# Kernel tuning notes

Measured on AMD Instinct MI355X. Metric: run time of the kernel, lower is better.

## Reference

```python
import jax, jax.numpy as jnp
import numpy as np
import math

C_S, C_Z, H, D, P_QK, P_V = 384, 128, 12, 16, 4, 8
B, L = 1, 512

def setup_inputs() -> dict:
    ks = jax.random.split(jax.random.key(0), 16)
    sc = lambda fan_in: 1.0 / math.sqrt(fan_in)
    return {
        's': jax.random.normal(ks[0], (B, L, C_S), jnp.float32),
        'z': jax.random.normal(ks[1], (B, L, L, C_Z), jnp.float32),
        'R': jax.random.normal(ks[2], (B, L, 3, 3), jnp.float32),
        't': jax.random.normal(ks[3], (B, L, 3), jnp.float32),
        'g_s': jnp.ones((C_S,), jnp.float32),
        'b_s': jnp.zeros((C_S,), jnp.float32),
        'g_z': jnp.ones((C_Z,), jnp.float32),
        'b_z': jnp.zeros((C_Z,), jnp.float32),
        'Wq': jax.random.normal(ks[4], (C_S, H * D), jnp.float32) * sc(C_S),
        'Wk': jax.random.normal(ks[5], (C_S, H * D), jnp.float32) * sc(C_S),
        'Wv': jax.random.normal(ks[6], (C_S, H * D), jnp.float32) * sc(C_S),
        'Wqp': jax.random.normal(ks[7], (C_S, H * P_QK * 3), jnp.float32) * sc(C_S),
        'Wkp': jax.random.normal(ks[8], (C_S, H * P_QK * 3), jnp.float32) * sc(C_S),
        'Wvp': jax.random.normal(ks[9], (C_S, H * P_V * 3), jnp.float32) * sc(C_S),
        'Wpb': jax.random.normal(ks[10], (C_Z, H), jnp.float32) * sc(C_Z),
        'pw': jax.random.normal(ks[11], (H,), jnp.float32) * 0.1,
        'Wo': jax.random.normal(ks[12], (H * D + H * P_V * 3 + H * P_V, C_S), jnp.float32) * sc(H * D + H * P_V * 3 + H * P_V),
        'bo': jnp.zeros((C_S,), jnp.float32),
    }

def _ln(x, g, b, eps=1e-5):
    mu = jnp.mean(x, axis=-1, keepdims=True)
    var = jnp.mean(jnp.square(x - mu), axis=-1, keepdims=True)
    return (x - mu) * jax.lax.rsqrt(var + eps) * g + b

def reference(s, z, R, t, g_s, b_s, g_z, b_z, Wq, Wk, Wv, Wqp, Wkp, Wvp, Wpb, pw, Wo, bo):
    Bn, Ln, _ = s.shape
    sn = _ln(s, g_s, b_s)
    zn = _ln(z, g_z, b_z)
    q_s = (sn @ Wq).reshape(Bn, Ln, H, D)
    k_s = (sn @ Wk).reshape(Bn, Ln, H, D)
    v_s = (sn @ Wv).reshape(Bn, Ln, H, D)
    q_pl = (sn @ Wqp).reshape(Bn, Ln, H, P_QK, 3)
    k_pl = (sn @ Wkp).reshape(Bn, Ln, H, P_QK, 3)
    v_pl = (sn @ Wvp).reshape(Bn, Ln, H, P_V, 3)
    # local->global frame transform: x_global = R x_local + t
    tb = t[:, :, None, None, :]
    q_p = jnp.einsum('blij,blhpj->blhpi', R, q_pl) + tb
    k_p = jnp.einsum('blij,blhpj->blhpi', R, k_pl) + tb
    v_p = jnp.einsum('blij,blhpj->blhpi', R, v_pl) + tb
    scalar_logits = jnp.einsum('bihd,bjhd->bijh', q_s, k_s) / math.sqrt(D)
    pair_logits = zn @ Wpb  # (B,L,L,H)
    # sum_p |q_ip - k_jp|^2 without materializing the (B,L,L,H,P,3) diff tensor
    qn2 = jnp.sum(jnp.square(q_p), axis=(-1, -2))  # (B,L,H)
    kn2 = jnp.sum(jnp.square(k_p), axis=(-1, -2))
    qk = jnp.einsum('bihpc,bjhpc->bijh', q_p, k_p)
    dist2 = qn2[:, :, None, :] + kn2[:, None, :, :] - 2.0 * qk
    w = jax.nn.softplus(pw)[None, None, None, :]
    logits = scalar_logits + pair_logits - 0.5 * w * dist2
    attn = jax.nn.softmax(logits, axis=2)  # over keys j
    out_s = jnp.einsum('bijh,bjhd->bihd', attn, v_s)
    out_pg = jnp.einsum('bijh,bjhpc->bihpc', attn, v_p)
    # global->local: R^T (x - t); (R^T)_{xy} = R_{yx}
    out_pl = jnp.einsum('blyx,blhpy->blhpx', R, out_pg - tb)
    out_pn = jnp.sqrt(jnp.sum(jnp.square(out_pl), axis=-1) + 1e-8)
    out_cat = jnp.concatenate([out_s.reshape(Bn, Ln, -1), out_pl.reshape(Bn, Ln, -1), out_pn.reshape(Bn, Ln, -1)], axis=-1)
    return s + out_cat @ Wo + bo
```

## Files before the change

kernel.cpp:

```cpp
#include <hip/hip_runtime.h>

typedef float f32x4 __attribute__((ext_vector_type(4)));
typedef short bf16x8 __attribute__((ext_vector_type(8)));
typedef unsigned short u16x4 __attribute__((ext_vector_type(4)));

#define MFMA16(a,b,c) __builtin_amdgcn_mfma_f32_16x16x32_bf16((a),(b),(c),0,0,0)

__device__ __forceinline__ unsigned short f2bf(float f){
  unsigned int u = __builtin_bit_cast(unsigned int, f);
  u += 0x7FFFu + ((u>>16)&1u);
  return (unsigned short)(u>>16);
}
__device__ __forceinline__ float bf2f(unsigned short u){
  return __builtin_bit_cast(float, ((unsigned int)u)<<16);
}

#define OFF_SNBF  0u
#define OFF_PROJ  393216u
#define OFF_QP    2752512u
#define OFF_KFRAG 3047424u
#define OFF_VFRAG 3440640u
#define OFF_KN2   4030464u
#define OFF_PLT   4055040u
#define OFF_OBUF  10346496u
#define OFF_CATBF 11329536u
#define OFF_WPBF  11919360u
#define OFF_GZF   11923456u
#define OFF_BZF   11931648u
#define OFF_WCF   11939840u
#define OFF_WOF   12824576u
#define OFF_WBUF  13266944u

__global__ __launch_bounds__(256) void k_prep(
    const float* __restrict__ s, const float* __restrict__ g_s, const float* __restrict__ b_s,
    unsigned short* __restrict__ snbf,
    const float* __restrict__ Wq, const float* __restrict__ Wk, const float* __restrict__ Wv,
    const float* __restrict__ Wqp, const float* __restrict__ Wkp, const float* __restrict__ Wvp,
    const float* __restrict__ Wpb, const float* __restrict__ pw, const float* __restrict__ Wo,
    const float* __restrict__ g_z, const float* __restrict__ b_z,
    unsigned short* __restrict__ wpbfrag, float* __restrict__ gzfrag, float* __restrict__ bzfrag,
    unsigned short* __restrict__ wcfrag, unsigned short* __restrict__ wofrag,
    float* __restrict__ wbuf){
  if (blockIdx.x < 128){
    int l = blockIdx.x*4 + (threadIdx.x>>6);
    int lane = threadIdx.x & 63;
    float v[6]; float sum=0.f, ss=0.f;
    #pragma unroll
    for (int k=0;k<6;k++){
      float x = s[l*384 + lane + 64*k];
      v[k]=x; sum += x; ss = fmaf(x,x,ss);
    }
    #pragma unroll
    for (int m=1;m<64;m<<=1){ sum += __shfl_xor(sum,m); ss += __shfl_xor(ss,m); }
    float mu = sum*(1.f/384.f);
    float var = ss*(1.f/384.f) - mu*mu;
    float rs = rsqrtf(var + 1e-5f);
    #pragma unroll
    for (int k=0;k<6;k++){
      int c = lane + 64*k;
      snbf[l*384 + c] = f2bf((v[k]-mu)*rs*g_s[c] + b_s[c]);
    }
    return;
  }
  int idx = (blockIdx.x-128)*256 + threadIdx.x;
  const int N_wpb = 2048, N_gz = 2048, N_wc = 72*12*64*8, N_wo = 24*18*64*8;
  if (idx < N_wpb){
    int r = idx&7, lane=(idx>>3)&63, chunk=idx>>9;
    int c = chunk*32 + ((lane>>4)<<3) + r; int h = lane&15;
    wpbfrag[idx] = (h<12) ? f2bf(Wpb[c*12+h]) : (unsigned short)0;
    return;
  }
  idx -= N_wpb;
  if (idx < N_gz){
    int r = idx&7, lane=(idx>>3)&63, chunk=idx>>9;
    int c = chunk*32 + ((lane>>4)<<3) + r;
    gzfrag[idx] = g_z[c]; bzfrag[idx] = b_z[c];
    return;
  }
  idx -= N_gz;
  if (idx < N_wc){
    int r = idx&7, lane=(idx>>3)&63, kt=(idx>>9)%12, nt=idx/(12*512);
    int k = kt*32 + ((lane>>4)<<3) + r; int n = nt*16 + (lane&15);
    float v;
    if      (n < 192) v = Wq [k*192 + n];
    else if (n < 384) v = Wk [k*192 + (n-192)];
    else if (n < 576) v = Wv [k*192 + (n-384)];
    else if (n < 720) v = Wqp[k*144 + (n-576)];
    else if (n < 864) v = Wkp[k*144 + (n-720)];
    else              v = Wvp[k*288 + (n-864)];
    wcfrag[idx] = f2bf(v);
    return;
  }
  idx -= N_wc;
  if (idx < N_wo){
    int r = idx&7, lane=(idx>>3)&63, kt=(idx>>9)%18, nt=idx/(18*512);
    int k = kt*32 + ((lane>>4)<<3) + r; int n = nt*16 + (lane&15);
    wofrag[idx] = f2bf(Wo[k*384 + n]);
    return;
  }
  idx -= N_wo;
  if (idx < 12){
    float x = pw[idx];
    wbuf[idx] = log1pf(expf(x));
  }
}

__global__ __launch_bounds__(256) void k_proj(const unsigned short* __restrict__ snbf,
    const unsigned short* __restrict__ wcfrag, float* __restrict__ proj){
  int wid = blockIdx.x*4 + (threadIdx.x>>6);
  int lane = threadIdx.x & 63;
  int il = lane&15, ig = lane>>4;
  int nt = wid % 72, ib = wid / 72;
  int i0 = ib*16;
  f32x4 acc = {0.f,0.f,0.f,0.f};
  #pragma unroll
  for (int kt=0; kt<12; kt++){
    bf16x8 a = *(const bf16x8*)(snbf + (i0+il)*384 + kt*32 + ig*8);
    bf16x8 b = *(const bf16x8*)(wcfrag + (size_t)((nt*12+kt)*64 + lane)*8);
    acc = MFMA16(a, b, acc);
  }
  #pragma unroll
  for (int r=0;r<4;r++)
    proj[(i0 + ig*4 + r)*1152 + nt*16 + il] = acc[r];
}

__global__ __launch_bounds__(192) void k_points(const float* __restrict__ proj,
    const float* __restrict__ Rm, const float* __restrict__ tv,
    float* __restrict__ qpb, unsigned short* __restrict__ kfrag,
    unsigned short* __restrict__ vfrag, float* __restrict__ kn2T){
  int l = blockIdx.x; int t = threadIdx.x;
  __shared__ float Rl[9], tl[3];
  __shared__ float kp_lds[12][12];
  __shared__ float vp_lds[12][24];
  __shared__ float kn2acc[12][4];
  if (t < 9) Rl[t] = Rm[l*9 + t];
  if (t < 3) tl[t] = tv[l*3 + t];
  __syncthreads();
  int h = t >> 4, pt = t & 15;
  {
    int ptype = (pt<4)? 0 : ((pt<8)? 1 : 2);
    int p = pt - ((ptype==0)?0:((ptype==1)?4:8));
    int col0 = (ptype==0)?576:((ptype==1)?720:864);
    int stride = (ptype==2)?24:12;
    const float* src = proj + l*1152 + col0 + h*stride + p*3;
    float lx=src[0], ly=src[1], lz=src[2];
    float cx = Rl[0]*lx + Rl[1]*ly + Rl[2]*lz + tl[0];
    float cy = Rl[3]*lx + Rl[4]*ly + Rl[5]*lz + tl[1];
    float cz = Rl[6]*lx + Rl[7]*ly + Rl[8]*lz + tl[2];
    if (ptype==0){
      float* d = qpb + (l*12 + h)*12 + p*3;
      d[0]=cx; d[1]=cy; d[2]=cz;
    } else if (ptype==1){
      kp_lds[h][p*3+0]=cx; kp_lds[h][p*3+1]=cy; kp_lds[h][p*3+2]=cz;
      kn2acc[h][p] = cx*cx + cy*cy + cz*cz;
    } else {
      vp_lds[h][p*3+0]=cx; vp_lds[h][p*3+1]=cy; vp_lds[h][p*3+2]=cz;
    }
  }
  __syncthreads();
  if (t < 12)
    kn2T[t*512 + l] = kn2acc[t][0]+kn2acc[t][1]+kn2acc[t][2]+kn2acc[t][3];
  {
    int jt = l >> 4, jl = l & 15;
    int q = pt >> 2, rr = (pt & 3)*2;
    unsigned short* dst = kfrag + (size_t)((h*32 + jt)*64 + 16*q + jl)*8 + rr;
    #pragma unroll
    for (int e=0;e<2;e++){
      int k = pt*2 + e; float f;
      if (k < 16)      f = proj[l*1152 + 192 + h*16 + k];
      else if (k < 28) f = kp_lds[h][k-16];
      else             f = 0.f;
      dst[e] = f2bf(f);
    }
  }
  {
    int d = pt; int jc = l >> 5; int jin = l & 31;
    int qq = (jin & 15) >> 2;
    int rr = (jin & 3) + ((jin >> 4) << 2);
    #pragma unroll
    for (int dt=0; dt<3; dt++){
      int dd = dt*16 + d; float f;
      if (dd < 16)      f = proj[l*1152 + 384 + h*16 + dd];
      else if (dd < 40) f = vp_lds[h][dd-16];
      else              f = 0.f;
      vfrag[(size_t)(((h*16 + jc)*3 + dt)*64 + 16*qq + d)*8 + rr] = f2bf(f);
    }
  }
}

__global__ __launch_bounds__(256) void k_pairbias(const float* __restrict__ z,
    const unsigned short* __restrict__ wpbfrag, const float* __restrict__ gzfrag,
    const float* __restrict__ bzfrag, unsigned short* __restrict__ plTbf){
  int w = blockIdx.x*4 + (threadIdx.x>>6);
  int lane = threadIdx.x & 63;
  int il = lane & 15, ig = lane >> 4;
  int nw = gridDim.x*4;
  f32x4 gzv[8], bzv[8];
  bf16x8 wf[4];
  #pragma unroll
  for (int c=0;c<4;c++){
    gzv[2*c]   = *(const f32x4*)(gzfrag + (c*64+lane)*8);
    gzv[2*c+1] = *(const f32x4*)(gzfrag + (c*64+lane)*8 + 4);
    bzv[2*c]   = *(const f32x4*)(bzfrag + (c*64+lane)*8);
    bzv[2*c+1] = *(const f32x4*)(bzfrag + (c*64+lane)*8 + 4);
    wf[c] = *(const bf16x8*)(wpbfrag + (c*64+lane)*8);
  }
  for (int g = w; g < 16384; g += nw){
    int j = g >> 5; int i0 = (g & 31) << 4;
    const float* zr = z + (size_t)((i0+il)*512 + j)*128;
    f32x4 zv[8];
    #pragma unroll
    for (int c=0;c<4;c++){
      zv[2*c]   = *(const f32x4*)(zr + c*32 + ig*8);
      zv[2*c+1] = *(const f32x4*)(zr + c*32 + ig*8 + 4);
    }
    float sum=0.f, ss=0.f;
    #pragma unroll
    for (int m=0;m<8;m++)
      #pragma unroll
      for (int e=0;e<4;e++){ float x = zv[m][e]; sum += x; ss = fmaf(x,x,ss); }
    sum += __shfl_xor(sum,16); sum += __shfl_xor(sum,32);
    ss  += __shfl_xor(ss,16);  ss  += __shfl_xor(ss,32);
    float mu  = sum*(1.f/128.f);
    float var = ss*(1.f/128.f) - mu*mu;
    float rs  = rsqrtf(var + 1e-5f);
    f32x4 acc = {0.f,0.f,0.f,0.f};
    #pragma unroll
    for (int c=0;c<4;c++){
      bf16x8 zf;
      #pragma unroll
      for (int r=0;r<8;r++){
        float gv = (r<4)? gzv[2*c][r&3] : gzv[2*c+1][r&3];
        float bv = (r<4)? bzv[2*c][r&3] : bzv[2*c+1][r&3];
        float xv = (r<4)? zv[2*c][r&3]  : zv[2*c+1][r&3];
        zf[r] = (short)f2bf((xv-mu)*(rs*gv) + bv);
      }
      acc = MFMA16(zf, wf[c], acc);
    }
    if (il < 12){
      u16x4 ov;
      #pragma unroll
      for (int r=0;r<4;r++) ov[r] = f2bf(acc[r]);
      *(u16x4*)(plTbf + (size_t)(il*512 + j)*512 + i0 + ig*4) = ov;
    }
  }
}

__global__ __launch_bounds__(512) void k_attn(const float* __restrict__ proj,
    const float* __restrict__ qpb, const float* __restrict__ wbuf,
    const unsigned short* __restrict__ kfrag, const unsigned short* __restrict__ plTbf,
    const float* __restrict__ kn2T, const unsigned short* __restrict__ vfrag,
    float* __restrict__ obuf){
  int u = blockIdx.x;
  int h = u % 12, ib = u / 12;
  int i0 = ib*16;
  int tid = threadIdx.x;
  int w = tid >> 6, lane = tid & 63;
  int il = lane & 15, ig = lane >> 4;
  __shared__ float red[8][16];
  __shared__ float gsum[16];
  __shared__ float osum[8][64][13];
  float wh = wbuf[h];
  float wneg = -0.5f*wh;
  bf16x8 qfrag;
  #pragma unroll
  for (int r=0;r<8;r++){
    int k = ig*8 + r; float f;
    if (k < 16)      f = proj[(i0+il)*1152 + h*16 + k]*0.25f;
    else if (k < 28) f = qpb[((i0+il)*12 + h)*12 + (k-16)]*wh;
    else             f = 0.f;
    qfrag[r] = (short)f2bf(f);
  }
  int jt0 = w*4;
  f32x4 sv[4];
  const unsigned short* kbase = kfrag + (size_t)(h*32)*64*8;
  const unsigned short* pbase = plTbf + (size_t)(h*512)*512;
  const float* kbn = kn2T + h*512;
  #pragma unroll
  for (int jj=0;jj<4;jj++){
    int jt = jt0+jj;
    bf16x8 kf = *(const bf16x8*)(kbase + (size_t)(jt*64 + lane)*8);
    f32x4 c0;
    #pragma unroll
    for (int r=0;r<4;r++){
      int j = jt*16 + ig*4 + r;
      c0[r] = bf2f(pbase[(size_t)j*512 + i0 + il]) + wneg*kbn[j];
    }
    sv[jj] = MFMA16(kf, qfrag, c0);
  }
  float mx = -3.0e38f;
  #pragma unroll
  for (int jj=0;jj<4;jj++){
    #pragma unroll
    for (int r=0;r<4;r++) mx = fmaxf(mx, sv[jj][r]);
  }
  mx = fmaxf(mx, __shfl_xor(mx,16));
  mx = fmaxf(mx, __shfl_xor(mx,32));
  if (lane < 16) red[w][lane] = mx;
  __syncthreads();
  float gm = red[0][il];
  #pragma unroll
  for (int ww=1;ww<8;ww++) gm = fmaxf(gm, red[ww][il]);
  __syncthreads();
  float sum = 0.f;
  #pragma unroll
  for (int jj=0;jj<4;jj++){
    #pragma unroll
    for (int r=0;r<4;r++){ float p = __expf(sv[jj][r]-gm); sv[jj][r]=p; sum+=p; }
  }
  sum += __shfl_xor(sum,16);
  sum += __shfl_xor(sum,32);
  if (lane < 16) red[w][lane] = sum;
  __syncthreads();
  float gs = 0.f;
  #pragma unroll
  for (int ww=0;ww<8;ww++) gs += red[ww][il];
  if (w == 0 && lane < 16) gsum[lane] = gs;
  f32x4 o0={0.f,0.f,0.f,0.f}, o1=o0, o2=o0;
  const unsigned short* vbase = vfrag + (size_t)(h*16)*3*64*8;
  #pragma unroll
  for (int jcl=0;jcl<2;jcl++){
    int jc = w*2 + jcl;
    bf16x8 pfrag;
    #pragma unroll
    for (int r=0;r<8;r++) pfrag[r] = (short)f2bf(sv[2*jcl + (r>>2)][r&3]);
    bf16x8 v0 = *(const bf16x8*)(vbase + (size_t)((jc*3+0)*64 + lane)*8);
    bf16x8 v1 = *(const bf16x8*)(vbase + (size_t)((jc*3+1)*64 + lane)*8);
    bf16x8 v2 = *(const bf16x8*)(vbase + (size_t)((jc*3+2)*64 + lane)*8);
    o0 = MFMA16(v0, pfrag, o0);
    o1 = MFMA16(v1, pfrag, o1);
    o2 = MFMA16(v2, pfrag, o2);
  }
  #pragma unroll
  for (int r=0;r<4;r++){
    osum[w][lane][r]   = o0[r];
    osum[w][lane][4+r] = o1[r];
    osum[w][lane][8+r] = o2[r];
  }
  __syncthreads();
  for (int idx = tid; idx < 640; idx += 512){
    int i = idx & 15, d = idx >> 4;
    int seg = d >> 4, dr = d & 15;
    int lx = ((dr>>2) << 4) + i;
    int c = seg*4 + (dr & 3);
    float v = 0.f;
    #pragma unroll
    for (int ww=0;ww<8;ww++) v += osum[ww][lx][c];
    obuf[(i0+i)*480 + h*40 + d] = v / gsum[i];
  }
}

__global__ __launch_bounds__(192) void k_cat(const float* __restrict__ obuf,
    const float* __restrict__ Rm, const float* __restrict__ tv,
    unsigned short* __restrict__ catbf){
  int l = blockIdx.x; int t = threadIdx.x;
  __shared__ float Rl[9], tl[3];
  if (t < 9) Rl[t] = Rm[l*9 + t];
  if (t < 3) tl[t] = tv[l*3 + t];
  __syncthreads();
  catbf[l*576 + t] = f2bf(obuf[l*480 + (t>>4)*40 + (t&15)]);
  if (t < 96){
    int hh = t >> 3, p = t & 7;
    float oy0 = obuf[l*480 + hh*40 + 16 + p*3 + 0] - tl[0];
    float oy1 = obuf[l*480 + hh*40 + 16 + p*3 + 1] - tl[1];
    float oy2 = obuf[l*480 + hh*40 + 16 + p*3 + 2] - tl[2];
    float px = Rl[0]*oy0 + Rl[3]*oy1 + Rl[6]*oy2;
    float py = Rl[1]*oy0 + Rl[4]*oy1 + Rl[7]*oy2;
    float pz = Rl[2]*oy0 + Rl[5]*oy1 + Rl[8]*oy2;
    catbf[l*576 + 192 + t*3 + 0] = f2bf(px);
    catbf[l*576 + 192 + t*3 + 1] = f2bf(py);
    catbf[l*576 + 192 + t*3 + 2] = f2bf(pz);
    catbf[l*576 + 480 + t] = f2bf(sqrtf(px*px + py*py + pz*pz + 1e-8f));
  }
}

__global__ __launch_bounds__(256) void k_outgemm(const unsigned short* __restrict__ catbf,
    const unsigned short* __restrict__ wofrag, const float* __restrict__ s,
    const float* __restrict__ bo, float* __restrict__ out){
  int wid = blockIdx.x*4 + (threadIdx.x>>6);
  int lane = threadIdx.x & 63;
  int il = lane&15, ig = lane>>4;
  int nt = wid % 24, ib = wid / 24;
  int i0 = ib*16;
  int n = nt*16 + il;
  f32x4 acc = {0.f,0.f,0.f,0.f};
  #pragma unroll
  for (int kt=0; kt<18; kt++){
    bf16x8 a = *(const bf16x8*)(catbf + (i0+il)*576 + kt*32 + ig*8);
    bf16x8 b = *(const bf16x8*)(wofrag + (size_t)((nt*18+kt)*64 + lane)*8);
    acc = MFMA16(a, b, acc);
  }
  float bv = bo[n];
  #pragma unroll
  for (int r=0;r<4;r++){
    int row = i0 + ig*4 + r;
    out[row*384 + n] = s[row*384 + n] + bv + acc[r];
  }
}

extern "C" void kernel_launch(void* const* d_in, const int* in_sizes, int n_in,
                              void* d_out, int out_size, void* d_ws, size_t ws_size,
                              hipStream_t stream) {
  const float* s   = (const float*)d_in[0];
  const float* z   = (const float*)d_in[1];
  const float* R   = (const float*)d_in[2];
  const float* t   = (const float*)d_in[3];
  const float* g_s = (const float*)d_in[4];
  const float* b_s = (const float*)d_in[5];
  const float* g_z = (const float*)d_in[6];
  const float* b_z = (const float*)d_in[7];
  const float* Wq  = (const float*)d_in[8];
  const float* Wk  = (const float*)d_in[9];
  const float* Wv  = (const float*)d_in[10];
  const float* Wqp = (const float*)d_in[11];
  const float* Wkp = (const float*)d_in[12];
  const float* Wvp = (const float*)d_in[13];
  const float* Wpb = (const float*)d_in[14];
  const float* pw  = (const float*)d_in[15];
  const float* Wo  = (const float*)d_in[16];
  const float* bo  = (const float*)d_in[17];
  float* out = (float*)d_out;
  char* ws = (char*)d_ws;

  unsigned short* snbf    = (unsigned short*)(ws + OFF_SNBF);
  float*          proj    = (float*)(ws + OFF_PROJ);
  float*          qpb     = (float*)(ws + OFF_QP);
  unsigned short* kfrag   = (unsigned short*)(ws + OFF_KFRAG);
  unsigned short* vfrag   = (unsigned short*)(ws + OFF_VFRAG);
  float*          kn2T    = (float*)(ws + OFF_KN2);
  unsigned short* plTbf   = (unsigned short*)(ws + OFF_PLT);
  float*          obuf    = (float*)(ws + OFF_OBUF);
  unsigned short* catbf   = (unsigned short*)(ws + OFF_CATBF);
  unsigned short* wpbfrag = (unsigned short*)(ws + OFF_WPBF);
  float*          gzfrag  = (float*)(ws + OFF_GZF);
  float*          bzfrag  = (float*)(ws + OFF_BZF);
  unsigned short* wcfrag  = (unsigned short*)(ws + OFF_WCF);
  unsigned short* wofrag  = (unsigned short*)(ws + OFF_WOF);
  float*          wbuf    = (float*)(ws + OFF_WBUF);

  k_prep<<<2737, 256, 0, stream>>>(s, g_s, b_s, snbf,
                                   Wq, Wk, Wv, Wqp, Wkp, Wvp, Wpb, pw, Wo, g_z, b_z,
                                   wpbfrag, gzfrag, bzfrag, wcfrag, wofrag, wbuf);
  k_proj<<<576, 256, 0, stream>>>(snbf, wcfrag, proj);
  k_points<<<512, 192, 0, stream>>>(proj, R, t, qpb, kfrag, vfrag, kn2T);
  k_pairbias<<<1024, 256, 0, stream>>>(z, wpbfrag, gzfrag, bzfrag, plTbf);
  k_attn<<<384, 512, 0, stream>>>(proj, qpb, wbuf, kfrag, plTbf, kn2T, vfrag, obuf);
  k_cat<<<512, 192, 0, stream>>>(obuf, R, t, catbf);
  k_outgemm<<<192, 256, 0, stream>>>(catbf, wofrag, s, bo, out);
}
```

Measured before the change: 61.04 us.

## Fuse all stages into one cooperative persistent kernel with grid syncs

```diff
diff --git a/kernel.cpp b/kernel.cpp
--- a/kernel.cpp
+++ b/kernel.cpp
@@ -1,8 +1,8 @@
 #include <hip/hip_runtime.h>
+#include <hip/hip_cooperative_groups.h>
 
 typedef float f32x4 __attribute__((ext_vector_type(4)));
 typedef short bf16x8 __attribute__((ext_vector_type(8)));
-typedef unsigned short u16x4 __attribute__((ext_vector_type(4)));
 
 #define MFMA16(a,b,c) __builtin_amdgcn_mfma_f32_16x16x32_bf16((a),(b),(c),0,0,0)
 
@@ -23,428 +23,422 @@
 #define OFF_KN2   4030464u
 #define OFF_PLT   4055040u
 #define OFF_OBUF  10346496u
-#define OFF_CATBF 11329536u
-#define OFF_WPBF  11919360u
-#define OFF_GZF   11923456u
-#define OFF_BZF   11931648u
-#define OFF_WCF   11939840u
-#define OFF_WOF   12824576u
-#define OFF_WBUF  13266944u
-
-__global__ __launch_bounds__(256) void k_prep(
-    const float* __restrict__ s, const float* __restrict__ g_s, const float* __restrict__ b_s,
-    unsigned short* __restrict__ snbf,
-    const float* __restrict__ Wq, const float* __restrict__ Wk, const float* __restrict__ Wv,
-    const float* __restrict__ Wqp, const float* __restrict__ Wkp, const float* __restrict__ Wvp,
-    const float* __restrict__ Wpb, const float* __restrict__ pw, const float* __restrict__ Wo,
+#define OFF_WCF   11329536u
+#define OFF_WOF   12214272u
+#define OFF_WBUF  12656640u
+
+struct MegaParams {
+  const float *s, *z, *R, *tv, *g_s, *b_s, *g_z, *b_z;
+  const float *Wq, *Wk, *Wv, *Wqp, *Wkp, *Wvp, *Wpb, *pw, *Wo, *bo;
+  float* out; char* ws; int G; int PB1;
+};
+
+__device__ __forceinline__ void pb_frags(const float* __restrict__ Wpb,
     const float* __restrict__ g_z, const float* __restrict__ b_z,
-    unsigned short* __restrict__ wpbfrag, float* __restrict__ gzfrag, float* __restrict__ bzfrag,
-    unsigned short* __restrict__ wcfrag, unsigned short* __restrict__ wofrag,
-    float* __restrict__ wbuf){
-  if (blockIdx.x < 128){
-    int l = blockIdx.x*4 + (threadIdx.x>>6);
-    int lane = threadIdx.x & 63;
-    float v[6]; float sum=0.f, ss=0.f;
-    #pragma unroll
-    for (int k=0;k<6;k++){
-      float x = s[l*384 + lane + 64*k];
-      v[k]=x; sum += x; ss = fmaf(x,x,ss);
-    }
-    #pragma unroll
-    for (int m=1;m<64;m<<=1){ sum += __shfl_xor(sum,m); ss += __shfl_xor(ss,m); }
-    float mu = sum*(1.f/384.f);
-    float var = ss*(1.f/384.f) - mu*mu;
-    float rs = rsqrtf(var + 1e-5f);
-    #pragma unroll
-    for (int k=0;k<6;k++){
-      int c = lane + 64*k;
-      snbf[l*384 + c] = f2bf((v[k]-mu)*rs*g_s[c] + b_s[c]);
-    }
-    return;
-  }
-  int idx = (blockIdx.x-128)*256 + threadIdx.x;
-  const int N_wpb = 2048, N_gz = 2048, N_wc = 72*12*64*8, N_wo = 24*18*64*8;
-  if (idx < N_wpb){
-    int r = idx&7, lane=(idx>>3)&63, chunk=idx>>9;
-    int c = chunk*32 + ((lane>>4)<<3) + r; int h = lane&15;
-    wpbfrag[idx] = (h<12) ? f2bf(Wpb[c*12+h]) : (unsigned short)0;
-    return;
-  }
-  idx -= N_wpb;
-  if (idx < N_gz){
-    int r = idx&7, lane=(idx>>3)&63, chunk=idx>>9;
-    int c = chunk*32 + ((lane>>4)<<3) + r;
-    gzfrag[idx] = g_z[c]; bzfrag[idx] = b_z[c];
-    return;
-  }
-  idx -= N_gz;
-  if (idx < N_wc){
-    int r = idx&7, lane=(idx>>3)&63, kt=(idx>>9)%12, nt=idx/(12*512);
-    int k = kt*32 + ((lane>>4)<<3) + r; int n = nt*16 + (lane&15);
-    float v;
-    if      (n < 192) v = Wq [k*192 + n];
-    else if (n < 384) v = Wk [k*192 + (n-192)];
-    else if (n < 576) v = Wv [k*192 + (n-384)];
-    else if (n < 720) v = Wqp[k*144 + (n-576)];
-    else if (n < 864) v = Wkp[k*144 + (n-720)];
-    else              v = Wvp[k*288 + (n-864)];
-    wcfrag[idx] = f2bf(v);
-    return;
-  }
-  idx -= N_wc;
-  if (idx < N_wo){
-    int r = idx&7, lane=(idx>>3)&63, kt=(idx>>9)%18, nt=idx/(18*512);
-    int k = kt*32 + ((lane>>4)<<3) + r; int n = nt*16 + (lane&15);
-    wofrag[idx] = f2bf(Wo[k*384 + n]);
-    return;
-  }
-  idx -= N_wo;
-  if (idx < 12){
-    float x = pw[idx];
-    wbuf[idx] = log1pf(expf(x));
-  }
-}
-
-__global__ __launch_bounds__(256) void k_proj(const unsigned short* __restrict__ snbf,
-    const unsigned short* __restrict__ wcfrag, float* __restrict__ proj){
-  int wid = blockIdx.x*4 + (threadIdx.x>>6);
-  int lane = threadIdx.x & 63;
-  int il = lane&15, ig = lane>>4;
-  int nt = wid % 72, ib = wid / 72;
-  int i0 = ib*16;
+    int il, int ig, bf16x8* gzb, bf16x8* bzb, bf16x8* wf){
+  #pragma unroll
+  for (int c=0;c<4;c++){
+    #pragma unroll
+    for (int r=0;r<8;r++){
+      int cc = c*32 + ig*8 + r;
+      gzb[c][r] = (short)f2bf(g_z[cc]);
+      bzb[c][r] = (short)f2bf(b_z[cc]);
+      wf[c][r]  = (il<12) ? (short)f2bf(Wpb[cc*12 + il]) : (short)0;
+    }
+  }
+}
+
+__device__ __forceinline__ void pb_unit(int g, const float* __restrict__ z,
+    unsigned short* __restrict__ plTbf, int il, int ig,
+    const bf16x8* gzb, const bf16x8* bzb, const bf16x8* wf){
+  int j = g >> 5; int i0 = (g & 31) << 4;
+  const float* zr = z + (size_t)((i0+il)*512 + j)*128;
+  f32x4 zv[8];
+  #pragma unroll
+  for (int c=0;c<4;c++){
+    zv[2*c]   = *(const f32x4*)(zr + c*32 + ig*8);
+    zv[2*c+1] = *(const f32x4*)(zr + c*32 + ig*8 + 4);
+  }
+  float sum=0.f, ss=0.f;
+  #pragma unroll
+  for (int m=0;m<8;m++)
+    #pragma unroll
+    for (int e=0;e<4;e++){ float x = zv[m][e]; sum += x; ss = fmaf(x,x,ss); }
+  sum += __shfl_xor(sum,16); sum += __shfl_xor(sum,32);
+  ss  += __shfl_xor(ss,16);  ss  += __shfl_xor(ss,32);
+  float mu  = sum*(1.f/128.f);
+  float var = ss*(1.f/128.f) - mu*mu;
+  float rs  = rsqrtf(var + 1e-5f);
   f32x4 acc = {0.f,0.f,0.f,0.f};
   #pragma unroll
-  for (int kt=0; kt<12; kt++){
-    bf16x8 a = *(const bf16x8*)(snbf + (i0+il)*384 + kt*32 + ig*8);
-    bf16x8 b = *(const bf16x8*)(wcfrag + (size_t)((nt*12+kt)*64 + lane)*8);
-    acc = MFMA16(a, b, acc);
-  }
-  #pragma unroll
-  for (int r=0;r<4;r++)
-    proj[(i0 + ig*4 + r)*1152 + nt*16 + il] = acc[r];
-}
-
-__global__ __launch_bounds__(192) void k_points(const float* __restrict__ proj,
-    const float* __restrict__ Rm, const float* __restrict__ tv,
-    float* __restrict__ qpb, unsigned short* __restrict__ kfrag,
-    unsigned short* __restrict__ vfrag, float* __restrict__ kn2T){
-  int l = blockIdx.x; int t = threadIdx.x;
-  __shared__ float Rl[9], tl[3];
-  __shared__ float kp_lds[12][12];
-  __shared__ float vp_lds[12][24];
-  __shared__ float kn2acc[12][4];
-  if (t < 9) Rl[t] = Rm[l*9 + t];
-  if (t < 3) tl[t] = tv[l*3 + t];
-  __syncthreads();
-  int h = t >> 4, pt = t & 15;
-  {
-    int ptype = (pt<4)? 0 : ((pt<8)? 1 : 2);
-    int p = pt - ((ptype==0)?0:((ptype==1)?4:8));
-    int col0 = (ptype==0)?576:((ptype==1)?720:864);
-    int stride = (ptype==2)?24:12;
-    const float* src = proj + l*1152 + col0 + h*stride + p*3;
-    float lx=src[0], ly=src[1], lz=src[2];
-    float cx = Rl[0]*lx + Rl[1]*ly + Rl[2]*lz + tl[0];
-    float cy = Rl[3]*lx + Rl[4]*ly + Rl[5]*lz + tl[1];
-    float cz = Rl[6]*lx + Rl[7]*ly + Rl[8]*lz + tl[2];
-    if (ptype==0){
-      float* d = qpb + (l*12 + h)*12 + p*3;
-      d[0]=cx; d[1]=cy; d[2]=cz;
-    } else if (ptype==1){
-      kp_lds[h][p*3+0]=cx; kp_lds[h][p*3+1]=cy; kp_lds[h][p*3+2]=cz;
-      kn2acc[h][p] = cx*cx + cy*cy + cz*cz;
-    } else {
-      vp_lds[h][p*3+0]=cx; vp_lds[h][p*3+1]=cy; vp_lds[h][p*3+2]=cz;
-    }
-  }
-  __syncthreads();
-  if (t < 12)
-    kn2T[t*512 + l] = kn2acc[t][0]+kn2acc[t][1]+kn2acc[t][2]+kn2acc[t][3];
-  {
-    int jt = l >> 4, jl = l & 15;
-    int q = pt >> 2, rr = (pt & 3)*2;
-    unsigned short* dst = kfrag + (size_t)((h*32 + jt)*64 + 16*q + jl)*8 + rr;
-    #pragma unroll
-    for (int e=0;e<2;e++){
-      int k = pt*2 + e; float f;
-      if (k < 16)      f = proj[l*1152 + 192 + h*16 + k];
-      else if (k < 28) f = kp_lds[h][k-16];
+  for (int c=0;c<4;c++){
+    bf16x8 zf;
+    #pragma unroll
+    for (int r=0;r<8;r++){
+      float xv = (r<4)? zv[2*c][r&3] : zv[2*c+1][r&3];
+      float gv = bf2f((unsigned short)gzb[c][r]);
+      float bv = bf2f((unsigned short)bzb[c][r]);
+      zf[r] = (short)f2bf((xv-mu)*(rs*gv) + bv);
+    }
+    acc = MFMA16(zf, wf[c], acc);
+  }
+  if (il < 12){
+    unsigned short o0=f2bf(acc[0]), o1=f2bf(acc[1]), o2=f2bf(acc[2]), o3=f2bf(acc[3]);
+    unsigned long long pk = (unsigned long long)o0 | ((unsigned long long)o1<<16)
+                          | ((unsigned long long)o2<<32) | ((unsigned long long)o3<<48);
+    *(unsigned long long*)(plTbf + (size_t)(il*512 + j)*512 + i0 + ig*4) = pk;
+  }
+}
+
+__global__ __launch_bounds__(256, 3) void k_mega(MegaParams P){
+  cooperative_groups::grid_group grid = cooperative_groups::this_grid();
+  const int bid = blockIdx.x, tid = threadIdx.x;
+  const int w = tid>>6, lane = tid&63, il = lane&15, ig = lane>>4;
+  char* ws = P.ws;
+  unsigned short* snbf  = (unsigned short*)(ws + OFF_SNBF);
+  float*          proj  = (float*)(ws + OFF_PROJ);
+  float*          qpb   = (float*)(ws + OFF_QP);
+  unsigned short* kfrag = (unsigned short*)(ws + OFF_KFRAG);
+  unsigned short* vfrag = (unsigned short*)(ws + OFF_VFRAG);
+  float*          kn2T  = (float*)(ws + OFF_KN2);
+  unsigned short* plTbf = (unsigned short*)(ws + OFF_PLT);
+  float*          obuf  = (float*)(ws + OFF_OBUF);
+  unsigned short* wcfrag= (unsigned short*)(ws + OFF_WCF);
+  unsigned short* wofrag= (unsigned short*)(ws + OFF_WOF);
+  float*          wbuf  = (float*)(ws + OFF_WBUF);
+
+  __shared__ union {
+    struct { float red[4][16]; float gsum[16]; float osum[4][64][13]; } a;
+    unsigned short cat[16*584];
+  } sm;
+
+  const int G = P.G, PB1 = P.PB1;
+
+  if (bid < PB1){
+    for (int u = bid; u < 189; u += PB1){
+      if (u < 24){
+        int k = u*16 + (tid>>4), nloc = tid & 15;
+        int kt = k>>5, kin = k&31;
+        int fl = (kin>>3)*16 + nloc, r = kin&7;
+        #pragma unroll 4
+        for (int nt=0; nt<72; nt++){
+          int n = nt*16 + nloc;
+          float v;
+          if      (n < 192) v = P.Wq [k*192 + n];
+          else if (n < 384) v = P.Wk [k*192 + (n-192)];
+          else if (n < 576) v = P.Wv [k*192 + (n-384)];
+          else if (n < 720) v = P.Wqp[k*144 + (n-576)];
+          else if (n < 864) v = P.Wkp[k*144 + (n-720)];
+          else              v = P.Wvp[k*288 + (n-864)];
+          wcfrag[((size_t)(nt*12+kt)*64 + fl)*8 + r] = f2bf(v);
+        }
+      } else if (u < 60){
+        int k = (u-24)*16 + (tid>>4), nloc = tid & 15;
+        int kt = k>>5, kin = k&31;
+        int fl = (kin>>3)*16 + nloc, r = kin&7;
+        #pragma unroll 4
+        for (int nt=0; nt<24; nt++){
+          int n = nt*16 + nloc;
+          wofrag[((size_t)(nt*18+kt)*64 + fl)*8 + r] = f2bf(P.Wo[k*384 + n]);
+        }
+      } else if (u < 188){
+        int l = (u-60)*4 + w;
+        float v[6]; float sum=0.f, ss=0.f;
+        #pragma unroll
+        for (int k=0;k<6;k++){
+          float x = P.s[l*384 + lane + 64*k];
+          v[k]=x; sum += x; ss = fmaf(x,x,ss);
+        }
+        #pragma unroll
+        for (int m=1;m<64;m<<=1){ sum += __shfl_xor(sum,m); ss += __shfl_xor(ss,m); }
+        float mu = sum*(1.f/384.f);
+        float var = ss*(1.f/384.f) - mu*mu;
+        float rs = rsqrtf(var + 1e-5f);
+        #pragma unroll
+        for (int k=0;k<6;k++){
+          int c = lane + 64*k;
+          snbf[l*384 + c] = f2bf((v[k]-mu)*rs*P.g_s[c] + P.b_s[c]);
+        }
+      } else {
+        if (tid < 12) wbuf[tid] = log1pf(expf(P.pw[tid]));
+      }
+    }
+  } else {
+    bf16x8 gzb[4], bzb[4], wf[4];
+    pb_frags(P.Wpb, P.g_z, P.b_z, il, ig, gzb, bzb, wf);
+    int wid1 = (bid-PB1)*4 + w;
+    int U1 = (G-PB1)*4; if (U1 > 16384) U1 = 16384;
+    if (wid1 < U1) pb_unit(wid1, P.z, plTbf, il, ig, gzb, bzb, wf);
+  }
+  grid.sync();
+
+  if (bid < 32){
+    int i0 = bid*16;
+    bf16x8 afr[12];
+    #pragma unroll
+    for (int kt=0;kt<12;kt++)
+      afr[kt] = *(const bf16x8*)(snbf + (i0+il)*384 + kt*32 + ig*8);
+    for (int nt = w; nt < 72; nt += 4){
+      f32x4 acc = {0.f,0.f,0.f,0.f};
+      #pragma unroll
+      for (int kt=0;kt<12;kt++){
+        bf16x8 b = *(const bf16x8*)(wcfrag + ((size_t)(nt*12+kt)*64 + lane)*8);
+        acc = MFMA16(afr[kt], b, acc);
+      }
+      #pragma unroll
+      for (int r=0;r<4;r++)
+        proj[(i0 + ig*4 + r)*1152 + nt*16 + il] = acc[r];
+    }
+    __threadfence();
+    __syncthreads();
+    if (tid < 192){
+      int rr = tid/12, h = tid - rr*12;
+      int l = i0 + rr;
+      float Rl[9], tl[3];
+      #pragma unroll
+      for (int e=0;e<9;e++) Rl[e] = P.R[l*9+e];
+      #pragma unroll
+      for (int e=0;e<3;e++) tl[e] = P.tv[l*3+e];
+      const float* prow = proj + (size_t)l*1152;
+      #pragma unroll
+      for (int p=0;p<4;p++){
+        float lx = prow[576 + h*12 + p*3+0];
+        float ly = prow[576 + h*12 + p*3+1];
+        float lz = prow[576 + h*12 + p*3+2];
+        qpb[((size_t)l*12+h)*12 + p*3+0] = Rl[0]*lx + Rl[1]*ly + Rl[2]*lz + tl[0];
+        qpb[((size_t)l*12+h)*12 + p*3+1] = Rl[3]*lx + Rl[4]*ly + Rl[5]*lz + tl[1];
+        qpb[((size_t)l*12+h)*12 + p*3+2] = Rl[6]*lx + Rl[7]*ly + Rl[8]*lz + tl[2];
+      }
+      float kp[12]; float kn2 = 0.f;
+      #pragma unroll
+      for (int p=0;p<4;p++){
+        float lx = prow[720 + h*12 + p*3+0];
+        float ly = prow[720 + h*12 + p*3+1];
+        float lz = prow[720 + h*12 + p*3+2];
+        float cx = Rl[0]*lx + Rl[1]*ly + Rl[2]*lz + tl[0];
+        float cy = Rl[3]*lx + Rl[4]*ly + Rl[5]*lz + tl[1];
+        float cz = Rl[6]*lx + Rl[7]*ly + Rl[8]*lz + tl[2];
+        kp[p*3+0]=cx; kp[p*3+1]=cy; kp[p*3+2]=cz;
+        kn2 += cx*cx + cy*cy + cz*cz;
+      }
+      kn2T[h*512 + l] = kn2;
+      {
+        int jt = l>>4, jl = l&15;
+        #pragma unroll
+        for (int k=0;k<32;k++){
+          float f = (k<16) ? prow[192 + h*16 + k] : ((k<28) ? kp[k-16] : 0.f);
+          kfrag[((size_t)(h*32+jt)*64 + 16*(k>>3) + jl)*8 + (k&7)] = f2bf(f);
+        }
+      }
+      float vp[24];
+      #pragma unroll
+      for (int p=0;p<8;p++){
+        float lx = prow[864 + h*24 + p*3+0];
+        float ly = prow[864 + h*24 + p*3+1];
+        float lz = prow[864 + h*24 + p*3+2];
+        vp[p*3+0] = Rl[0]*lx + Rl[1]*ly + Rl[2]*lz + tl[0];
+        vp[p*3+1] = Rl[3]*lx + Rl[4]*ly + Rl[5]*lz + tl[1];
+        vp[p*3+2] = Rl[6]*lx + Rl[7]*ly + Rl[8]*lz + tl[2];
+      }
+      {
+        int jc = l>>5, jin = l&31;
+        int qq = (jin&15)>>2;
+        int rv = (jin&3) + ((jin>>4)<<2);
+        #pragma unroll
+        for (int dd=0;dd<48;dd++){
+          float f = (dd<16) ? prow[384 + h*16 + dd] : ((dd<40) ? vp[dd-16] : 0.f);
+          int dt = dd>>4, d_ = dd&15;
+          vfrag[((size_t)((h*16+jc)*3+dt)*64 + 16*qq + d_)*8 + rv] = f2bf(f);
+        }
+      }
+    }
+  } else {
+    bf16x8 gzb[4], bzb[4], wf[4];
+    pb_frags(P.Wpb, P.g_z, P.b_z, il, ig, gzb, bzb, wf);
+    int U1 = (G-PB1)*4; if (U1 > 16384) U1 = 16384;
+    int W2 = (G-32)*4;
+    int wid2 = (bid-32)*4 + w;
+    for (int u = U1 + wid2; u < 16384; u += W2)
+      pb_unit(u, P.z, plTbf, il, ig, gzb, bzb, wf);
+  }
+  grid.sync();
+
+  for (int u = bid; u < 384; u += G){
+    int h = u % 12, ib = u / 12;
+    int i0 = ib*16;
+    float wh = wbuf[h];
+    float wneg = -0.5f*wh;
+    bf16x8 qfrag;
+    #pragma unroll
+    for (int r=0;r<8;r++){
+      int k = ig*8 + r; float f;
+      if (k < 16)      f = proj[(size_t)(i0+il)*1152 + h*16 + k]*0.25f;
+      else if (k < 28) f = qpb[((size_t)(i0+il)*12 + h)*12 + (k-16)]*wh;
       else             f = 0.f;
-      dst[e] = f2bf(f);
-    }
-  }
-  {
-    int d = pt; int jc = l >> 5; int jin = l & 31;
-    int qq = (jin & 15) >> 2;
-    int rr = (jin & 3) + ((jin >> 4) << 2);
-    #pragma unroll
-    for (int dt=0; dt<3; dt++){
-      int dd = dt*16 + d; float f;
-      if (dd < 16)      f = proj[l*1152 + 384 + h*16 + dd];
-      else if (dd < 40) f = vp_lds[h][dd-16];
-      else              f = 0.f;
-      vfrag[(size_t)(((h*16 + jc)*3 + dt)*64 + 16*qq + d)*8 + rr] = f2bf(f);
-    }
-  }
-}
-
-__global__ __launch_bounds__(256) void k_pairbias(const float* __restrict__ z,
-    const unsigned short* __restrict__ wpbfrag, const float* __restrict__ gzfrag,
-    const float* __restrict__ bzfrag, unsigned short* __restrict__ plTbf){
-  int w = blockIdx.x*4 + (threadIdx.x>>6);
-  int lane = threadIdx.x & 63;
-  int il = lane & 15, ig = lane >> 4;
-  int nw = gridDim.x*4;
-  f32x4 gzv[8], bzv[8];
-  bf16x8 wf[4];
-  #pragma unroll
-  for (int c=0;c<4;c++){
-    gzv[2*c]   = *(const f32x4*)(gzfrag + (c*64+lane)*8);
-    gzv[2*c+1] = *(const f32x4*)(gzfrag + (c*64+lane)*8 + 4);
-    bzv[2*c]   = *(const f32x4*)(bzfrag + (c*64+lane)*8);
-    bzv[2*c+1] = *(const f32x4*)(bzfrag + (c*64+lane)*8 + 4);
-    wf[c] = *(const bf16x8*)(wpbfrag + (c*64+lane)*8);
-  }
-  for (int g = w; g < 16384; g += nw){
-    int j = g >> 5; int i0 = (g & 31) << 4;
-    const float* zr = z + (size_t)((i0+il)*512 + j)*128;
-    f32x4 zv[8];
-    #pragma unroll
-    for (int c=0;c<4;c++){
-      zv[2*c]   = *(const f32x4*)(zr + c*32 + ig*8);
-      zv[2*c+1] = *(const f32x4*)(zr + c*32 + ig*8 + 4);
-    }
-    float sum=0.f, ss=0.f;
-    #pragma unroll
-    for (int m=0;m<8;m++)
-      #pragma unroll
-      for (int e=0;e<4;e++){ float x = zv[m][e]; sum += x; ss = fmaf(x,x,ss); }
-    sum += __shfl_xor(sum,16); sum += __shfl_xor(sum,32);
-    ss  += __shfl_xor(ss,16);  ss  += __shfl_xor(ss,32);
-    float mu  = sum*(1.f/128.f);
-    float var = ss*(1.f/128.f) - mu*mu;
-    float rs  = rsqrtf(var + 1e-5f);
-    f32x4 acc = {0.f,0.f,0.f,0.f};
-    #pragma unroll
-    for (int c=0;c<4;c++){
-      bf16x8 zf;
-      #pragma unroll
-      for (int r=0;r<8;r++){
-        float gv = (r<4)? gzv[2*c][r&3] : gzv[2*c+1][r&3];
-        float bv = (r<4)? bzv[2*c][r&3] : bzv[2*c+1][r&3];
-        float xv = (r<4)? zv[2*c][r&3]  : zv[2*c+1][r&3];
-        zf[r] = (short)f2bf((xv-mu)*(rs*gv) + bv);
-      }
-      acc = MFMA16(zf, wf[c], acc);
-    }
-    if (il < 12){
-      u16x4 ov;
-      #pragma unroll
-      for (int r=0;r<4;r++) ov[r] = f2bf(acc[r]);
-      *(u16x4*)(plTbf + (size_t)(il*512 + j)*512 + i0 + ig*4) = ov;
-    }
-  }
-}
-
-__global__ __launch_bounds__(512) void k_attn(const float* __restrict__ proj,
-    const float* __restrict__ qpb, const float* __restrict__ wbuf,
-    const unsigned short* __restrict__ kfrag, const unsigned short* __restrict__ plTbf,
-    const float* __restrict__ kn2T, const unsigned short* __restrict__ vfrag,
-    float* __restrict__ obuf){
-  int u = blockIdx.x;
-  int h = u % 12, ib = u / 12;
-  int i0 = ib*16;
-  int tid = threadIdx.x;
-  int w = tid >> 6, lane = tid & 63;
-  int il = lane & 15, ig = lane >> 4;
-  __shared__ float red[8][16];
-  __shared__ float gsum[16];
-  __shared__ float osum[8][64][13];
-  float wh = wbuf[h];
-  float wneg = -0.5f*wh;
-  bf16x8 qfrag;
-  #pragma unroll
-  for (int r=0;r<8;r++){
-    int k = ig*8 + r; float f;
-    if (k < 16)      f = proj[(i0+il)*1152 + h*16 + k]*0.25f;
-    else if (k < 28) f = qpb[((i0+il)*12 + h)*12 + (k-16)]*wh;
-    else             f = 0.f;
-    qfrag[r] = (short)f2bf(f);
-  }
-  int jt0 = w*4;
-  f32x4 sv[4];
-  const unsigned short* kbase = kfrag + (size_t)(h*32)*64*8;
-  const unsigned short* pbase = plTbf + (size_t)(h*512)*512;
-  const float* kbn = kn2T + h*512;
-  #pragma unroll
-  for (int jj=0;jj<4;jj++){
-    int jt = jt0+jj;
-    bf16x8 kf = *(const bf16x8*)(kbase + (size_t)(jt*64 + lane)*8);
-    f32x4 c0;
+      qfrag[r] = (short)f2bf(f);
+    }
+    f32x4 sv[8];
+    const unsigned short* kbase = kfrag + (size_t)(h*32)*512;
+    const unsigned short* pbase = plTbf + (size_t)h*512*512;
+    const float* kbn = kn2T + h*512;
+    #pragma unroll
+    for (int jj=0;jj<8;jj++){
+      int jt = w*8 + jj;
+      bf16x8 kf = *(const bf16x8*)(kbase + (size_t)(jt*64 + lane)*8);
+      f32x4 c0;
+      #pragma unroll
+      for (int r=0;r<4;r++){
+        int j = jt*16 + ig*4 + r;
+        c0[r] = bf2f(pbase[(size_t)j*512 + i0 + il]) + wneg*kbn[j];
+      }
+      sv[jj] = MFMA16(kf, qfrag, c0);
+    }
+    float mx = -3.0e38f;
+    #pragma unroll
+    for (int jj=0;jj<8;jj++)
+      #pragma unroll
+      for (int r=0;r<4;r++) mx = fmaxf(mx, sv[jj][r]);
+    mx = fmaxf(mx, __shfl_xor(mx,16));
+    mx = fmaxf(mx, __shfl_xor(mx,32));
+    if (lane < 16) sm.a.red[w][lane] = mx;
+    __syncthreads();
+    float gm = sm.a.red[0][il];
+    #pragma unroll
+    for (int ww=1;ww<4;ww++) gm = fmaxf(gm, sm.a.red[ww][il]);
+    __syncthreads();
+    float sum = 0.f;
+    #pragma unroll
+    for (int jj=0;jj<8;jj++)
+      #pragma unroll
+      for (int r=0;r<4;r++){ float p = __expf(sv[jj][r]-gm); sv[jj][r]=p; sum+=p; }
+    sum += __shfl_xor(sum,16);
+    sum += __shfl_xor(sum,32);
+    if (lane < 16) sm.a.red[w][lane] = sum;
+    __syncthreads();
+    float gs = 0.f;
+    #pragma unroll
+    for (int ww=0;ww<4;ww++) gs += sm.a.red[ww][il];
+    if (w == 0 && lane < 16) sm.a.gsum[lane] = gs;
+    f32x4 o0={0.f,0.f,0.f,0.f}, o1=o0, o2=o0;
+    const unsigned short* vbase = vfrag + (size_t)(h*16)*3*512;
+    #pragma unroll
+    for (int jcl=0;jcl<4;jcl++){
+      int jc = w*4 + jcl;
+      bf16x8 pfrag;
+      #pragma unroll
+      for (int r=0;r<8;r++) pfrag[r] = (short)f2bf(sv[2*jcl + (r>>2)][r&3]);
+      bf16x8 v0 = *(const bf16x8*)(vbase + (size_t)((jc*3+0)*64 + lane)*8);
+      bf16x8 v1 = *(const bf16x8*)(vbase + (size_t)((jc*3+1)*64 + lane)*8);
+      bf16x8 v2 = *(const bf16x8*)(vbase + (size_t)((jc*3+2)*64 + lane)*8);
+      o0 = MFMA16(v0, pfrag, o0);
+      o1 = MFMA16(v1, pfrag, o1);
+      o2 = MFMA16(v2, pfrag, o2);
+    }
     #pragma unroll
     for (int r=0;r<4;r++){
-      int j = jt*16 + ig*4 + r;
-      c0[r] = bf2f(pbase[(size_t)j*512 + i0 + il]) + wneg*kbn[j];
-    }
-    sv[jj] = MFMA16(kf, qfrag, c0);
-  }
-  float mx = -3.0e38f;
-  #pragma unroll
-  for (int jj=0;jj<4;jj++){
-    #pragma unroll
-    for (int r=0;r<4;r++) mx = fmaxf(mx, sv[jj][r]);
-  }
-  mx = fmaxf(mx, __shfl_xor(mx,16));
-  mx = fmaxf(mx, __shfl_xor(mx,32));
-  if (lane < 16) red[w][lane] = mx;
-  __syncthreads();
-  float gm = red[0][il];
-  #pragma unroll
-  for (int ww=1;ww<8;ww++) gm = fmaxf(gm, red[ww][il]);
-  __syncthreads();
-  float sum = 0.f;
-  #pragma unroll
-  for (int jj=0;jj<4;jj++){
-    #pragma unroll
-    for (int r=0;r<4;r++){ float p = __expf(sv[jj][r]-gm); sv[jj][r]=p; sum+=p; }
-  }
-  sum += __shfl_xor(sum,16);
-  sum += __shfl_xor(sum,32);
-  if (lane < 16) red[w][lane] = sum;
-  __syncthreads();
-  float gs = 0.f;
-  #pragma unroll
-  for (int ww=0;ww<8;ww++) gs += red[ww][il];
-  if (w == 0 && lane < 16) gsum[lane] = gs;
-  f32x4 o0={0.f,0.f,0.f,0.f}, o1=o0, o2=o0;
-  const unsigned short* vbase = vfrag + (size_t)(h*16)*3*64*8;
-  #pragma unroll
-  for (int jcl=0;jcl<2;jcl++){
-    int jc = w*2 + jcl;
-    bf16x8 pfrag;
-    #pragma unroll
-    for (int r=0;r<8;r++) pfrag[r] = (short)f2bf(sv[2*jcl + (r>>2)][r&3]);
-    bf16x8 v0 = *(const bf16x8*)(vbase + (size_t)((jc*3+0)*64 + lane)*8);
-    bf16x8 v1 = *(const bf16x8*)(vbase + (size_t)((jc*3+1)*64 + lane)*8);
-    bf16x8 v2 = *(const bf16x8*)(vbase + (size_t)((jc*3+2)*64 + lane)*8);
-    o0 = MFMA16(v0, pfrag, o0);
-    o1 = MFMA16(v1, pfrag, o1);
-    o2 = MFMA16(v2, pfrag, o2);
-  }
-  #pragma unroll
-  for (int r=0;r<4;r++){
-    osum[w][lane][r]   = o0[r];
-    osum[w][lane][4+r] = o1[r];
-    osum[w][lane][8+r] = o2[r];
-  }
-  __syncthreads();
-  for (int idx = tid; idx < 640; idx += 512){
-    int i = idx & 15, d = idx >> 4;
-    int seg = d >> 4, dr = d & 15;
-    int lx = ((dr>>2) << 4) + i;
-    int c = seg*4 + (dr & 3);
-    float v = 0.f;
-    #pragma unroll
-    for (int ww=0;ww<8;ww++) v += osum[ww][lx][c];
-    obuf[(i0+i)*480 + h*40 + d] = v / gsum[i];
-  }
-}
-
-__global__ __launch_bounds__(192) void k_cat(const float* __restrict__ obuf,
-    const float* __restrict__ Rm, const float* __restrict__ tv,
-    unsigned short* __restrict__ catbf){
-  int l = blockIdx.x; int t = threadIdx.x;
-  __shared__ float Rl[9], tl[3];
-  if (t < 9) Rl[t] = Rm[l*9 + t];
-  if (t < 3) tl[t] = tv[l*3 + t];
-  __syncthreads();
-  catbf[l*576 + t] = f2bf(obuf[l*480 + (t>>4)*40 + (t&15)]);
-  if (t < 96){
-    int hh = t >> 3, p = t & 7;
-    float oy0 = obuf[l*480 + hh*40 + 16 + p*3 + 0] - tl[0];
-    float oy1 = obuf[l*480 + hh*40 + 16 + p*3 + 1] - tl[1];
-    float oy2 = obuf[l*480 + hh*40 + 16 + p*3 + 2] - tl[2];
-    float px = Rl[0]*oy0 + Rl[3]*oy1 + Rl[6]*oy2;
-    float py = Rl[1]*oy0 + Rl[4]*oy1 + Rl[7]*oy2;
-    float pz = Rl[2]*oy0 + Rl[5]*oy1 + Rl[8]*oy2;
-    catbf[l*576 + 192 + t*3 + 0] = f2bf(px);
-    catbf[l*576 + 192 + t*3 + 1] = f2bf(py);
-    catbf[l*576 + 192 + t*3 + 2] = f2bf(pz);
-    catbf[l*576 + 480 + t] = f2bf(sqrtf(px*px + py*py + pz*pz + 1e-8f));
-  }
-}
-
-__global__ __launch_bounds__(256) void k_outgemm(const unsigned short* __restrict__ catbf,
-    const unsigned short* __restrict__ wofrag, const float* __restrict__ s,
-    const float* __restrict__ bo, float* __restrict__ out){
-  int wid = blockIdx.x*4 + (threadIdx.x>>6);
-  int lane = threadIdx.x & 63;
-  int il = lane&15, ig = lane>>4;
-  int nt = wid % 24, ib = wid / 24;
-  int i0 = ib*16;
-  int n = nt*16 + il;
-  f32x4 acc = {0.f,0.f,0.f,0.f};
-  #pragma unroll
-  for (int kt=0; kt<18; kt++){
-    bf16x8 a = *(const bf16x8*)(catbf + (i0+il)*576 + kt*32 + ig*8);
-    bf16x8 b = *(const bf16x8*)(wofrag + (size_t)((nt*18+kt)*64 + lane)*8);
-    acc = MFMA16(a, b, acc);
-  }
-  float bv = bo[n];
-  #pragma unroll
-  for (int r=0;r<4;r++){
-    int row = i0 + ig*4 + r;
-    out[row*384 + n] = s[row*384 + n] + bv + acc[r];
+      sm.a.osum[w][lane][r]   = o0[r];
+      sm.a.osum[w][lane][4+r] = o1[r];
+      sm.a.osum[w][lane][8+r] = o2[r];
+    }
+    __syncthreads();
+    for (int idx = tid; idx < 640; idx += 256){
+      int i = idx & 15, d = idx >> 4;
+      int seg = d >> 4, dr = d & 15;
+      int lx = ((dr>>2) << 4) + i;
+      int c = seg*4 + (dr & 3);
+      float v = 0.f;
+      #pragma unroll
+      for (int ww=0;ww<4;ww++) v += sm.a.osum[ww][lx][c];
+      obuf[(size_t)(i0+i)*480 + h*40 + d] = v / sm.a.gsum[i];
+    }
+    __syncthreads();
+  }
+  grid.sync();
+
+  for (int u = bid; u < 32; u += G){
+    int i0 = u*16;
+    __syncthreads();
+    if (tid < 192){
+      int rr = tid/12, h = tid - rr*12;
+      int l = i0 + rr;
+      float Rl[9], tl[3];
+      #pragma unroll
+      for (int e=0;e<9;e++) Rl[e] = P.R[l*9+e];
+      #pragma unroll
+      for (int e=0;e<3;e++) tl[e] = P.tv[l*3+e];
+      const float* orow = obuf + (size_t)l*480 + h*40;
+      #pragma unroll
+      for (int d=0;d<16;d++) sm.cat[rr*584 + h*16 + d] = f2bf(orow[d]);
+      #pragma unroll
+      for (int p=0;p<8;p++){
+        float oy0 = orow[16 + p*3 + 0] - tl[0];
+        float oy1 = orow[16 + p*3 + 1] - tl[1];
+        float oy2 = orow[16 + p*3 + 2] - tl[2];
+        float px = Rl[0]*oy0 + Rl[3]*oy1 + Rl[6]*oy2;
+        float py = Rl[1]*oy0 + Rl[4]*oy1 + Rl[7]*oy2;
+        float pz = Rl[2]*oy0 + Rl[5]*oy1 + Rl[8]*oy2;
+        int cb = 192 + (h*8+p)*3;
+        sm.cat[rr*584 + cb+0] = f2bf(px);
+        sm.cat[rr*584 + cb+1] = f2bf(py);
+        sm.cat[rr*584 + cb+2] = f2bf(pz);
+        sm.cat[rr*584 + 480 + h*8 + p] = f2bf(sqrtf(px*px + py*py + pz*pz + 1e-8f));
+      }
+    }
+    __syncthreads();
+    for (int nt = w; nt < 24; nt += 4){
+      int n = nt*16 + il;
+      f32x4 acc = {0.f,0.f,0.f,0.f};
+      #pragma unroll
+      for (int kt=0;kt<18;kt++){
+        bf16x8 a = *(const bf16x8*)(&sm.cat[il*584 + kt*32 + ig*8]);
+        bf16x8 b = *(const bf16x8*)(wofrag + ((size_t)(nt*18+kt)*64 + lane)*8);
+        acc = MFMA16(a, b, acc);
+      }
+      float bv = P.bo[n];
+      #pragma unroll
+      for (int r=0;r<4;r++){
+        int row = i0 + ig*4 + r;
+        P.out[(size_t)row*384 + n] = P.s[(size_t)row*384 + n] + bv + acc[r];
+      }
+    }
   }
 }
 
 extern "C" void kernel_launch(void* const* d_in, const int* in_sizes, int n_in,
                               void* d_out, int out_size, void* d_ws, size_t ws_size,
                               hipStream_t stream) {
-  const float* s   = (const float*)d_in[0];
-  const float* z   = (const float*)d_in[1];
-  const float* R   = (const float*)d_in[2];
-  const float* t   = (const float*)d_in[3];
-  const float* g_s = (const float*)d_in[4];
-  const float* b_s = (const float*)d_in[5];
-  const float* g_z = (const float*)d_in[6];
-  const float* b_z = (const float*)d_in[7];
-  const float* Wq  = (const float*)d_in[8];
-  const float* Wk  = (const float*)d_in[9];
-  const float* Wv  = (const float*)d_in[10];
-  const float* Wqp = (const float*)d_in[11];
-  const float* Wkp = (const float*)d_in[12];
-  const float* Wvp = (const float*)d_in[13];
-  const float* Wpb = (const float*)d_in[14];
-  const float* pw  = (const float*)d_in[15];
-  const float* Wo  = (const float*)d_in[16];
-  const float* bo  = (const float*)d_in[17];
-  float* out = (float*)d_out;
-  char* ws = (char*)d_ws;
-
-  unsigned short* snbf    = (unsigned short*)(ws + OFF_SNBF);
-  float*          proj    = (float*)(ws + OFF_PROJ);
-  float*          qpb     = (float*)(ws + OFF_QP);
-  unsigned short* kfrag   = (unsigned short*)(ws + OFF_KFRAG);
-  unsigned short* vfrag   = (unsigned short*)(ws + OFF_VFRAG);
-  float*          kn2T    = (float*)(ws + OFF_KN2);
-  unsigned short* plTbf   = (unsigned short*)(ws + OFF_PLT);
-  float*          obuf    = (float*)(ws + OFF_OBUF);
-  unsigned short* catbf   = (unsigned short*)(ws + OFF_CATBF);
-  unsigned short* wpbfrag = (unsigned short*)(ws + OFF_WPBF);
-  float*          gzfrag  = (float*)(ws + OFF_GZF);
-  float*          bzfrag  = (float*)(ws + OFF_BZF);
-  unsigned short* wcfrag  = (unsigned short*)(ws + OFF_WCF);
-  unsigned short* wofrag  = (unsigned short*)(ws + OFF_WOF);
-  float*          wbuf    = (float*)(ws + OFF_WBUF);
-
-  k_prep<<<2737, 256, 0, stream>>>(s, g_s, b_s, snbf,
-                                   Wq, Wk, Wv, Wqp, Wkp, Wvp, Wpb, pw, Wo, g_z, b_z,
-                                   wpbfrag, gzfrag, bzfrag, wcfrag, wofrag, wbuf);
-  k_proj<<<576, 256, 0, stream>>>(snbf, wcfrag, proj);
-  k_points<<<512, 192, 0, stream>>>(proj, R, t, qpb, kfrag, vfrag, kn2T);
-  k_pairbias<<<1024, 256, 0, stream>>>(z, wpbfrag, gzfrag, bzfrag, plTbf);
-  k_attn<<<384, 512, 0, stream>>>(proj, qpb, wbuf, kfrag, plTbf, kn2T, vfrag, obuf);
-  k_cat<<<512, 192, 0, stream>>>(obuf, R, t, catbf);
-  k_outgemm<<<192, 256, 0, stream>>>(catbf, wofrag, s, bo, out);
-}
+  MegaParams prm;
+  prm.s   = (const float*)d_in[0];
+  prm.z   = (const float*)d_in[1];
+  prm.R   = (const float*)d_in[2];
+  prm.tv  = (const float*)d_in[3];
+  prm.g_s = (const float*)d_in[4];
+  prm.b_s = (const float*)d_in[5];
+  prm.g_z = (const float*)d_in[6];
+  prm.b_z = (const float*)d_in[7];
+  prm.Wq  = (const float*)d_in[8];
+  prm.Wk  = (const float*)d_in[9];
+  prm.Wv  = (const float*)d_in[10];
+  prm.Wqp = (const float*)d_in[11];
+  prm.Wkp = (const float*)d_in[12];
+  prm.Wvp = (const float*)d_in[13];
+  prm.Wpb = (const float*)d_in[14];
+  prm.pw  = (const float*)d_in[15];
+  prm.Wo  = (const float*)d_in[16];
+  prm.bo  = (const float*)d_in[17];
+  prm.out = (float*)d_out;
+  prm.ws  = (char*)d_ws;
+
+  int perCU = 0;
+  (void)hipOccupancyMaxActiveBlocksPerMultiprocessor(&perCU, k_mega, 256, 0);
+  int G = perCU * 256;
+  if (G > 768) G = 768;
+  if (G < 256) G = 256;
+  int PB1 = 192;
+  if (PB1 > G/2) PB1 = G/2;
+  prm.G = G;
+  prm.PB1 = PB1;
+
+  void* args[] = { &prm };
+  hipLaunchCooperativeKernel((void*)k_mega, dim3(G), dim3(256), args, 0, stream);
+}
```

Measured after the change: 204.1 us. 234% more time.
